# Kernel optimization log

Hardware: AMD Instinct MI355X
Metric: run time of the kernel (lower is better)

## Reference

```python
import jax, jax.numpy as jnp
import numpy as np
from jax import lax

K, E, HID, NH, L = 512, 256, 512, 8, 2
N, S1, S2, C, U, V, W = 2, 8, 9, 3, 8, 8, 8
S = S1 + S2 - 1  # 16, matches sum(cfg['seq_length']) - 1


def setup_inputs() -> dict:
    key = jax.random.key(0)
    ks = iter(jax.random.split(key, 40))
    g = lambda shape, s=0.02: jax.random.normal(next(ks), shape, jnp.float32) * s
    inp = {
        'code': jax.random.randint(next(ks), (N, S1, C, U, V, W), 0, K),
        'ncode': jax.random.randint(next(ks), (N, S2, C, U, V, W), 0, K),
        'emb': g((K, E)), 'pos_emb': g((S, E)),
        'Wq': g((L, 3, 3, 3, E, E)), 'bq': g((L, E)),
        'Wk': g((L, 3, 3, 3, E, E)), 'bk': g((L, E)),
        'Wv': g((L, 3, 3, 3, E, E)), 'bv': g((L, E)),
        'Wo': g((L, 3, 3, 3, E, E)), 'bo': g((L, E)),
        'ln1_g': jnp.ones((L, E)), 'ln1_b': jnp.zeros((L, E)),
        'ln2_g': jnp.ones((L, E)), 'ln2_b': jnp.zeros((L, E)),
        'Wc1': g((L, 3, 3, 3, E, HID)), 'bc1': g((L, HID)),
        'Wc2': g((L, 3, 3, 3, HID, E)), 'bc2': g((L, E)),
        'cls_W1': g((E, E)), 'cls_b1': jnp.zeros((E,)),
        'cls_ln_g': jnp.ones((E,)), 'cls_ln_b': jnp.zeros((E,)),
        'cls_W2': g((E, K)), 'cls_b2': jnp.zeros((K,)),
    }
    return inp


def _conv3d(t, w, b):
    # t: [B, S, U, V, W, Cin]; conv with kernel 3, stride 1, pad 1 (SAME)
    B_, S_, U_, V_, W_, Ci = t.shape
    y = lax.conv_general_dilated(t.reshape(B_ * S_, U_, V_, W_, Ci), w, (1, 1, 1), 'SAME',
                                 dimension_numbers=('NDHWC', 'DHWIO', 'NDHWC')) + b
    return y.reshape(B_, S_, U_, V_, W_, -1)


def _ln(t, g, b):
    mu = t.mean(-1, keepdims=True)
    var = ((t - mu) ** 2).mean(-1, keepdims=True)
    return (t - mu) * lax.rsqrt(var + 1e-5) * g + b


def _forward(code, ncode, emb, pos_emb, Wq, bq, Wk, bk, Wv, bv, Wo, bo,
             ln1_g, ln1_b, ln2_g, ln2_b, Wc1, bc1, Wc2, bc2,
             cls_W1, cls_b1, cls_ln_g, cls_ln_b, cls_W2, cls_b2):
    x = jnp.concatenate([code, ncode[:, :-1]], axis=1)  # [N, S, C, U, V, W]
    n, s, c, u, v, w = x.shape
    s2 = ncode.shape[1]
    x = x.transpose(0, 2, 1, 3, 4, 5).reshape(n * c, s, u, v, w)
    h = emb[x] + pos_emb[:s][None, :, None, None, None, :]  # [B, S, U, V, W, E]
    e = h.shape[-1]
    d = e // NH
    scale = jnp.asarray(d, h.dtype) ** 0.5
    # causal mask with first seq_length[0] columns fully visible
    m = jnp.tril(jnp.ones((s, s), bool)).at[:, :S1].set(True)

    def heads(t):
        return t.reshape(t.shape[0], s, u, v, w, NH, d).transpose(0, 5, 2, 3, 4, 1, 6)

    for i in range(Wq.shape[0]):
        q = heads(_conv3d(h, Wq[i], bq[i]))
        kk = heads(_conv3d(h, Wk[i], bk[i]))
        vv = heads(_conv3d(h, Wv[i], bv[i]))
        scores = jnp.einsum('bnuvwsd,bnuvwtd->bnuvwst', q, kk) / scale
        scores = jnp.where(m, scores, jnp.asarray(-1e30, scores.dtype))
        attn = jax.nn.softmax(scores, axis=-1)
        o = jnp.einsum('bnuvwst,bnuvwtd->bnuvwsd', attn, vv)
        o = o.transpose(0, 5, 2, 3, 4, 1, 6).reshape(h.shape[0], s, u, v, w, e)
        o = _conv3d(o, Wo[i], bo[i])
        h = _ln(h + o, ln1_g[i], ln1_b[i])
        f = _conv3d(jax.nn.gelu(_conv3d(h, Wc1[i], bc1[i]), approximate=False), Wc2[i], bc2[i])
        h = _ln(h + f, ln2_g[i], ln2_b[i])

    h = h[:, -s2:]
    h = h.reshape(n, c, s2, u, v, w, e).transpose(0, 2, 1, 3, 4, 5, 6)  # [N, S2, C, U, V, W, E]
    z = jnp.einsum('...e,ef->...f', h, cls_W1) + cls_b1
    z = jax.nn.gelu(_ln(z, cls_ln_g, cls_ln_b), approximate=False)
    z = jnp.einsum('...e,ek->...k', z, cls_W2) + cls_b2
    score = z.transpose(0, 6, 1, 2, 3, 4, 5)  # [N, K, S2, C, U, V, W]
    return score


def reference(code, ncode, emb, pos_emb, Wq, bq, Wk, bk, Wv, bv, Wo, bo,
              ln1_g, ln1_b, ln2_g, ln2_b, Wc1, bc1, Wc2, bc2,
              cls_W1, cls_b1, cls_ln_g, cls_ln_b, cls_W2, cls_b2):
    score = _forward(code, ncode, emb, pos_emb, Wq, bq, Wk, bk, Wv, bv, Wo, bo,
                     ln1_g, ln1_b, ln2_g, ln2_b, Wc1, bc1, Wc2, bc2,
                     cls_W1, cls_b1, cls_ln_g, cls_ln_b, cls_W2, cls_b2)
    logp = jax.nn.log_softmax(score, axis=1)
    nll = -jnp.take_along_axis(logp, ncode[:, None], axis=1)[:, 0]
    loss = nll.mean()
    pred = jnp.argmax(score, axis=1)
    return score, loss, pred
```

## Files before the change

kernel.cpp:

```cpp
#include <hip/hip_runtime.h>


typedef _Float16 f16;
typedef __attribute__((ext_vector_type(8))) _Float16 f16x8;
typedef __attribute__((ext_vector_type(4))) _Float16 f16x4;
typedef __attribute__((ext_vector_type(4))) float f32x4;

static constexpr long kSC = 14155776;
static constexpr float kDS = 4.8828125e-4f;

#define MFMA16(a, b, c) __builtin_amdgcn_mfma_f32_16x16x32_f16((a), (b), (c), 0, 0, 0)

__device__ __forceinline__ void gl16(const void* g, void* l) {
  __builtin_amdgcn_global_load_lds((const __attribute__((address_space(1))) void*)g,
                                   (__attribute__((address_space(3))) void*)l,
                                   16, 0, 0);
}

__device__ __forceinline__ float wave_sum_f(float x) {
#pragma unroll
  for (int m = 32; m; m >>= 1) x += __shfl_xor(x, m);
  return x;
}

__device__ __forceinline__ void split2(float x, f16* h, f16* l) {
  f16 hh = (f16)x;
  *h = hh;
  *l = (f16)((x - (float)hh) * 2048.0f);
}

__device__ __forceinline__ float rec2(f16 h, f16 l) {
  return (float)h + (float)l * kDS;
}

__device__ __forceinline__ float gelu_exact(float x) {
  return 0.5f * x * (1.0f + erff(x * 0.70710678118654752f));
}

__global__ __launch_bounds__(256) void wsplit_kernel(
    const float* __restrict__ src, f16* __restrict__ hi, f16* __restrict__ lo,
    int G, int Ci, int Co, int CoTot, int co0) {
  long n = (long)G * Ci * Co;
  long i = (long)blockIdx.x * 256 + threadIdx.x;
  if (i >= n) return;
  int co = (int)(i % Co);
  long t = i / Co;
  int ci = (int)(t % Ci);
  int g  = (int)(t / Ci);
  float x = src[i];
  long o = ((long)g * CoTot + co0 + co) * Ci + ci;
  split2(x, hi + o, lo + o);
}

__global__ __launch_bounds__(256) void bpack_kernel(
    const float* __restrict__ bq, const float* __restrict__ bk,
    const float* __restrict__ bv, float* __restrict__ dst) {
  int i = blockIdx.x * 256 + threadIdx.x;
  if (i < 256) dst[i] = bq[i];
  else if (i < 512) dst[i] = bk[i - 256];
  else if (i < 768) dst[i] = bv[i - 512];
}

__global__ __launch_bounds__(256) void embed_kernel(
    const int* __restrict__ code, const int* __restrict__ ncode,
    const float* __restrict__ emb, const float* __restrict__ pos,
    f16* __restrict__ Hh, f16* __restrict__ Hl) {
  int tok = blockIdx.x;
  int e = threadIdx.x;
  int g = tok >> 13;
  int rem = tok & 8191;
  int s = rem >> 9;
  int vox = rem & 511;
  int n = g / 3, c = g - 3 * n;
  int idx;
  if (s < 8) idx = code[((n * 8 + s) * 3 + c) * 512 + vox];
  else       idx = ncode[((n * 9 + (s - 8)) * 3 + c) * 512 + vox];
  float val = emb[idx * 256 + e] + pos[s * 256 + e];
  long o = (long)tok * 256 + e;
  split2(val, Hh + o, Hl + o);
}

template <int CIN, int COUTT, int ACT, int RESID>
__global__ __launch_bounds__(256, 2) void conv8_kernel(
    const f16* __restrict__ Xh, const f16* __restrict__ Xl, long xz_s, int xr,
    const f16* __restrict__ Wh, const f16* __restrict__ Wl,
    const float* __restrict__ bias,
    f16* __restrict__ Yh, f16* __restrict__ Yl, long yz_s, int yr, int nz) {
  constexpr int KB = CIN / 32;
  constexpr int NY = COUTT / 128;
  __shared__ __align__(16) f16 lsAll[40960];

  const int nwg = 64 * NY * nz;
  const int q = nwg >> 3;
  const int bid = blockIdx.x;
  const int wg = (bid & 7) * q + (bid >> 3);
  const int y = wg / (64 * nz);
  const int rem = wg - y * (64 * nz);
  const int z = rem >> 6;
  const int mt = rem & 63;
  const int img = mt >> 2, up = mt & 3;
  const int u0 = up * 2;
  const int coutb0 = y * 128;

  const int tid = threadIdx.x;
  const int wid = tid >> 6, lane = tid & 63;
  const int wm = wid >> 1, wn = wid & 1;
  const int l15 = lane & 15, lk = lane >> 4;

  const long xz = (long)z * xz_s;
  const long yz = (long)z * yz_s;

  f32x4 aA[4][4], aB[4][4];
#pragma unroll
  for (int mf = 0; mf < 4; ++mf)
#pragma unroll
    for (int nf = 0; nf < 4; ++nf) {
      float bv = bias[coutb0 + wn * 64 + nf * 16 + l15];
      aA[mf][nf] = (f32x4){bv, bv, bv, bv};
      aB[mf][nf] = (f32x4){0.f, 0.f, 0.f, 0.f};
    }

  const int swrow = tid >> 2;
  const int sswz = (tid & 3) ^ ((tid >> 3) & 3);

  auto stageA = [&](int kb) {
#pragma unroll
    for (int j = 0; j < 4; ++j) {
      const int uu = u0 - 1 + j;
      if (uu < 0 || uu >= 8) continue;
      const long g = xz + ((long)(img * 512 + uu * 64 + swrow)) * (long)xr
                     + kb * 32 + sswz * 8;
      gl16(Xh + g, &lsAll[j * 2048 + tid * 8]);
      gl16(Xl + g, &lsAll[8192 + j * 2048 + tid * 8]);
    }
  };
  auto stageB = [&](int o, int kb, int buf) {
    const int wb = 16384 + buf * 8192;
#pragma unroll
    for (int i = 0; i < 2; ++i) {
      const long g = ((long)o * COUTT + coutb0 + i * 64 + swrow) * (long)CIN
                     + kb * 32 + sswz * 8;
      gl16(Wh + g, &lsAll[wb + i * 2048 + tid * 8]);
      gl16(Wl + g, &lsAll[wb + 4096 + i * 2048 + tid * 8]);
    }
  };
  auto compute = [&](int o, int buf) {
    const int du = o / 9 - 1, dv = (o / 3) % 3 - 1, dw = o % 3 - 1;
    const int gu = u0 + wm + du;
    if ((unsigned)gu >= 8u) return;
    const int p = wm + 1 + du;
    const int wb = 16384 + buf * 8192;
    f16x8 bh[4], bl[4];
#pragma unroll
    for (int nf = 0; nf < 4; ++nf) {
      const int rb = wn * 64 + nf * 16 + l15;
      const int sw = lk ^ ((rb >> 1) & 3);
      bh[nf] = *(const f16x8*)&lsAll[wb + rb * 32 + sw * 8];
      bl[nf] = *(const f16x8*)&lsAll[wb + 4096 + rb * 32 + sw * 8];
    }
    __builtin_amdgcn_s_setprio(1);
#pragma unroll
    for (int mf = 0; mf < 4; ++mf) {
      const int vrow = mf * 16 + l15;
      const int vv = (vrow >> 3) + dv, ww = (vrow & 7) + dw;
      const bool ok = ((unsigned)vv < 8u) && ((unsigned)ww < 8u);
      f16x8 ah = {0, 0, 0, 0, 0, 0, 0, 0};
      f16x8 al = {0, 0, 0, 0, 0, 0, 0, 0};
      if (ok) {
        const int lrow = p * 64 + vv * 8 + ww;
        const int sw = lk ^ ((lrow >> 1) & 3);
        ah = *(const f16x8*)&lsAll[lrow * 32 + sw * 8];
        al = *(const f16x8*)&lsAll[8192 + lrow * 32 + sw * 8];
      }
#pragma unroll
      for (int nf = 0; nf < 4; ++nf) {
        aA[mf][nf] = MFMA16(ah, bh[nf], aA[mf][nf]);
        aB[mf][nf] = MFMA16(ah, bl[nf], aB[mf][nf]);
        aB[mf][nf] = MFMA16(al, bh[nf], aB[mf][nf]);
      }
    }
    __builtin_amdgcn_s_setprio(0);
  };

  stageA(0);
  stageB(0, 0, 0);

  int bcur = 0;
#pragma unroll 1
  for (int kb = 0; kb < KB; ++kb) {
#pragma unroll 1
    for (int o = 0; o < 27; ++o) {
      int bnext = bcur + 1; if (bnext == 3) bnext = 0;
      const bool haveNext = !(o == 26 && kb + 1 == KB);
      if (o < 26)           stageB(o + 1, kb, bnext);
      else if (kb + 1 < KB) stageB(0, kb + 1, bnext);
      if (haveNext) asm volatile("s_waitcnt vmcnt(4)\n\ts_barrier" ::: "memory");
      else          asm volatile("s_waitcnt vmcnt(0)\n\ts_barrier" ::: "memory");
      compute(o, bcur);
      if (o == 26 && kb + 1 < KB) {
        asm volatile("s_barrier" ::: "memory");
        stageA(kb + 1);
      }
      bcur = bnext;
    }
  }
  __syncthreads();

  float* sY = (float*)lsAll;
#pragma unroll 1
  for (int rh = 0; rh < 2; ++rh) {
    if (wm == rh) {
#pragma unroll
      for (int mf = 0; mf < 4; ++mf)
#pragma unroll
        for (int nf = 0; nf < 4; ++nf)
#pragma unroll
          for (int j = 0; j < 4; ++j) {
            const int row = mf * 16 + lk * 4 + j;
            const int col = wn * 64 + nf * 16 + l15;
            sY[row * 132 + col] = aA[mf][nf][j] + aB[mf][nf][j] * kDS;
          }
    }
    __syncthreads();
#pragma unroll
    for (int it = 0; it < 2; ++it) {
      const int row = it * 32 + (tid >> 3);
      const int c0 = (tid & 7) * 16;
      const long grow = (long)img * 512 + (u0 + rh) * 64 + row;
      const long gidx = yz + grow * (long)yr + coutb0 + c0;
      float yv[16];
#pragma unroll
      for (int i2 = 0; i2 < 16; ++i2) yv[i2] = sY[row * 132 + c0 + i2];
      if (ACT) {
#pragma unroll
        for (int i2 = 0; i2 < 16; ++i2) yv[i2] = gelu_exact(yv[i2]);
      }
      if (RESID) {
        f16x8 r0h = *(const f16x8*)&Yh[gidx];
        f16x8 r1h = *(const f16x8*)&Yh[gidx + 8];
        f16x8 r0l = *(const f16x8*)&Yl[gidx];
        f16x8 r1l = *(const f16x8*)&Yl[gidx + 8];
#pragma unroll
        for (int i2 = 0; i2 < 8; ++i2) {
          yv[i2] += rec2(r0h[i2], r0l[i2]);
          yv[8 + i2] += rec2(r1h[i2], r1l[i2]);
        }
      }
      f16x8 h0, h1, l0, l1;
#pragma unroll
      for (int i2 = 0; i2 < 8; ++i2) {
        f16 a, b;
        split2(yv[i2], &a, &b); h0[i2] = a; l0[i2] = b;
        split2(yv[8 + i2], &a, &b); h1[i2] = a; l1[i2] = b;
      }
      if (RESID) {
        *(f16x8*)&Yh[gidx] = h0;
        *(f16x8*)&Yh[gidx + 8] = h1;
        *(f16x8*)&Yl[gidx] = l0;
        *(f16x8*)&Yl[gidx + 8] = l1;
      } else {
        __builtin_nontemporal_store(h0, (f16x8*)&Yh[gidx]);
        __builtin_nontemporal_store(h1, (f16x8*)&Yh[gidx + 8]);
        __builtin_nontemporal_store(l0, (f16x8*)&Yl[gidx]);
        __builtin_nontemporal_store(l1, (f16x8*)&Yl[gidx + 8]);
      }
    }
    __syncthreads();
  }
}

template <int K_, int COUT, bool F32OUT>
__global__ __launch_bounds__(256) void gemm_kernel(
    const f16* __restrict__ Xh, const f16* __restrict__ Xl,
    const f16* __restrict__ Wh, const f16* __restrict__ Wl,
    const float* __restrict__ bias,
    f16* __restrict__ Yh, f16* __restrict__ Yl, float* __restrict__ Yf) {
  const int m0 = blockIdx.x * 64;
  const int coutb = blockIdx.y * 64;
  const int tid = threadIdx.x;
  const int wid = tid >> 6, lane = tid & 63;
  const int l15 = lane & 15, lk = lane >> 4;
  const int arow = m0 + wid * 16 + l15;

  f32x4 accA[4], accB[4];
#pragma unroll
  for (int cg = 0; cg < 4; ++cg) {
    float bv = bias[coutb + cg * 16 + l15];
    accA[cg] = (f32x4){bv, bv, bv, bv};
    accB[cg] = (f32x4){0.f, 0.f, 0.f, 0.f};
  }
  const f16* pah = Xh + (long)arow * K_ + lk * 8;
  const f16* pal = Xl + (long)arow * K_ + lk * 8;
  const f16* pbh = Wh + ((long)coutb + l15) * K_ + lk * 8;
  const f16* pbl = Wl + ((long)coutb + l15) * K_ + lk * 8;
#pragma unroll 2
  for (int kb = 0; kb < K_ / 32; ++kb) {
    f16x8 ah = *(const f16x8*)(pah + kb * 32);
    f16x8 al = *(const f16x8*)(pal + kb * 32);
#pragma unroll
    for (int cg = 0; cg < 4; ++cg) {
      f16x8 bh = *(const f16x8*)(pbh + (long)cg * 16 * K_ + kb * 32);
      f16x8 bl = *(const f16x8*)(pbl + (long)cg * 16 * K_ + kb * 32);
      accA[cg] = MFMA16(ah, bh, accA[cg]);
      accB[cg] = MFMA16(ah, bl, accB[cg]);
      accB[cg] = MFMA16(al, bh, accB[cg]);
    }
  }
  const long ybase = ((long)m0 + wid * 16) * (long)COUT + coutb;
#pragma unroll
  for (int cg = 0; cg < 4; ++cg)
#pragma unroll
    for (int j = 0; j < 4; ++j) {
      int r = lk * 4 + j;
      float y = accA[cg][j] + accB[cg][j] * kDS;
      long idx = ybase + (long)r * COUT + cg * 16 + l15;
      if (F32OUT) Yf[idx] = y;
      else        split2(y, Yh + idx, Yl + idx);
    }
}

__global__ __launch_bounds__(256) void attn_kernel(
    f16* __restrict__ QKVh, f16* __restrict__ QKVl) {
  __shared__ float sq[4][16][33];
  __shared__ float sk[4][16][33];
  __shared__ float sv[4][16][33];
  __shared__ float ss[4][16][17];
  const int wid = threadIdx.x >> 6, lane = threadIdx.x & 63;
  const int p = blockIdx.x * 4 + wid;
  const int cs = p >> 12;
  const int loc = p & 4095;
  const int nh = loc >> 9;
  const int vox = loc & 511;
  const int srow = lane >> 2;
  const int dp = (lane & 3) * 8;
  const long sbase = (long)cs * 6291456;
  const long base = sbase + ((long)(srow * 512 + vox)) * 768 + nh * 32 + dp;

  {
    f16x8 qh = *(const f16x8*)(QKVh + base);
    f16x8 ql = *(const f16x8*)(QKVl + base);
    f16x8 kh = *(const f16x8*)(QKVh + base + 256);
    f16x8 kl = *(const f16x8*)(QKVl + base + 256);
    f16x8 vh = *(const f16x8*)(QKVh + base + 512);
    f16x8 vl = *(const f16x8*)(QKVl + base + 512);
#pragma unroll
    for (int j = 0; j < 8; ++j) {
      sq[wid][srow][dp + j] = rec2(qh[j], ql[j]);
      sk[wid][srow][dp + j] = rec2(kh[j], kl[j]);
      sv[wid][srow][dp + j] = rec2(vh[j], vl[j]);
    }
  }
  __syncthreads();
#pragma unroll
  for (int pp = 0; pp < 4; ++pp) {
    int pr = lane * 4 + pp;
    int qi = pr >> 4, kt = pr & 15;
    float s = 0.f;
#pragma unroll
    for (int d = 0; d < 32; ++d) s += sq[wid][qi][d] * sk[wid][kt][d];
    bool allowed = (kt < 8) || (kt <= qi);
    ss[wid][qi][kt] = allowed ? s * 0.17677669529663687f : -1e30f;
  }
  __syncthreads();
  if (lane < 16) {
    float m = -1e30f;
#pragma unroll
    for (int t = 0; t < 16; ++t) m = fmaxf(m, ss[wid][lane][t]);
    float ex[16];
    float sum = 0.f;
#pragma unroll
    for (int t = 0; t < 16; ++t) { ex[t] = expf(ss[wid][lane][t] - m); sum += ex[t]; }
    float inv = 1.0f / sum;
#pragma unroll
    for (int t = 0; t < 16; ++t) ss[wid][lane][t] = ex[t] * inv;
  }
  __syncthreads();
  float o[8] = {0, 0, 0, 0, 0, 0, 0, 0};
#pragma unroll
  for (int t = 0; t < 16; ++t) {
    float a = ss[wid][srow][t];
#pragma unroll
    for (int j = 0; j < 8; ++j) o[j] += a * sv[wid][t][dp + j];
  }
#pragma unroll
  for (int j = 0; j < 8; ++j) split2(o[j], QKVh + base + j, QKVl + base + j);
}

__global__ __launch_bounds__(256) void ln_kernel(
    f16* __restrict__ Hh, f16* __restrict__ Hl,
    const float* __restrict__ gam, const float* __restrict__ bet) {
  const int wid = threadIdx.x >> 6, lane = threadIdx.x & 63;
  const long tok = (long)blockIdx.x * 4 + wid;
  const long base = tok * 256 + lane * 4;
  f16x4 hh = *(const f16x4*)(Hh + base);
  f16x4 hl = *(const f16x4*)(Hl + base);
  float v0 = rec2(hh[0], hl[0]), v1 = rec2(hh[1], hl[1]);
  float v2 = rec2(hh[2], hl[2]), v3 = rec2(hh[3], hl[3]);
  float mu = wave_sum_f(v0 + v1 + v2 + v3) * (1.0f / 256.0f);
  float d0 = v0 - mu, d1 = v1 - mu, d2 = v2 - mu, d3 = v3 - mu;
  float var = wave_sum_f(d0 * d0 + d1 * d1 + d2 * d2 + d3 * d3) * (1.0f / 256.0f);
  float rs = rsqrtf(var + 1e-5f);
  float4 gv = *(const float4*)(gam + lane * 4);
  float4 bv = *(const float4*)(bet + lane * 4);
  float y0 = d0 * rs * gv.x + bv.x, y1 = d1 * rs * gv.y + bv.y;
  float y2 = d2 * rs * gv.z + bv.z, y3 = d3 * rs * gv.w + bv.w;
  f16x4 oh, ol;
  f16 a, b2;
  split2(y0, &a, &b2); oh[0] = a; ol[0] = b2;
  split2(y1, &a, &b2); oh[1] = a; ol[1] = b2;
  split2(y2, &a, &b2); oh[2] = a; ol[2] = b2;
  split2(y3, &a, &b2); oh[3] = a; ol[3] = b2;
  *(f16x4*)(Hh + base) = oh;
  *(f16x4*)(Hl + base) = ol;
}

__global__ __launch_bounds__(256) void ln_gelu_kernel(
    f16* __restrict__ Zh, f16* __restrict__ Zl,
    const float* __restrict__ gam, const float* __restrict__ bet) {
  const int wid = threadIdx.x >> 6, lane = threadIdx.x & 63;
  const long tok = (long)blockIdx.x * 4 + wid;
  const long base = tok * 256 + lane * 4;
  f16x4 hh = *(const f16x4*)(Zh + base);
  f16x4 hl = *(const f16x4*)(Zl + base);
  float v0 = rec2(hh[0], hl[0]), v1 = rec2(hh[1], hl[1]);
  float v2 = rec2(hh[2], hl[2]), v3 = rec2(hh[3], hl[3]);
  float mu = wave_sum_f(v0 + v1 + v2 + v3) * (1.0f / 256.0f);
  float d0 = v0 - mu, d1 = v1 - mu, d2 = v2 - mu, d3 = v3 - mu;
  float var = wave_sum_f(d0 * d0 + d1 * d1 + d2 * d2 + d3 * d3) * (1.0f / 256.0f);
  float rs = rsqrtf(var + 1e-5f);
  float4 gv = *(const float4*)(gam + lane * 4);
  float4 bv = *(const float4*)(bet + lane * 4);
  float y0 = gelu_exact(d0 * rs * gv.x + bv.x);
  float y1 = gelu_exact(d1 * rs * gv.y + bv.y);
  float y2 = gelu_exact(d2 * rs * gv.z + bv.z);
  float y3 = gelu_exact(d3 * rs * gv.w + bv.w);
  f16x4 oh, ol;
  f16 a, b2;
  split2(y0, &a, &b2); oh[0] = a; ol[0] = b2;
  split2(y1, &a, &b2); oh[1] = a; ol[1] = b2;
  split2(y2, &a, &b2); oh[2] = a; ol[2] = b2;
  split2(y3, &a, &b2); oh[3] = a; ol[3] = b2;
  *(f16x4*)(Zh + base) = oh;
  *(f16x4*)(Zl + base) = ol;
}

__global__ __launch_bounds__(256) void gather_kernel(
    const f16* __restrict__ Hh, const f16* __restrict__ Hl, int n,
    f16* __restrict__ Xh, f16* __restrict__ Xl) {
  const int tc = blockIdx.x;
  const int e = threadIdx.x;
  const int s2 = tc / 1536;
  int r = tc - s2 * 1536;
  const int c = r >> 9;
  const int vox = r & 511;
  const int g = n * 3 + c;
  const int s = 7 + s2;
  const long src = ((long)(g * 16 + s) * 512 + vox) * 256 + e;
  const long dst = (long)tc * 256 + e;
  Xh[dst] = Hh[src];
  Xl[dst] = Hl[src];
}

__global__ __launch_bounds__(256) void transpose_kernel(
    const float* __restrict__ Z2, float* __restrict__ out) {
  __shared__ float tile[32][33];
  const int t0 = blockIdx.x * 32;
  const int k0 = blockIdx.y * 32;
  const int tx = threadIdx.x & 31;
  const int ty = threadIdx.x >> 5;
#pragma unroll
  for (int i = 0; i < 32; i += 8)
    tile[ty + i][tx] = Z2[((long)(t0 + ty + i)) * 512 + k0 + tx];
  __syncthreads();
#pragma unroll
  for (int i = 0; i < 32; i += 8)
    out[((long)(k0 + ty + i)) * 13824 + t0 + tx] = tile[tx][ty + i];
}

__global__ __launch_bounds__(256) void loss_pred_kernel(
    const float* __restrict__ Z2, const int* __restrict__ ncode,
    float* __restrict__ pred, float* __restrict__ partial) {
  __shared__ float sh[4];
  const int wid = threadIdx.x >> 6, lane = threadIdx.x & 63;
  const int tok = blockIdx.x * 4 + wid;
  const float* row = Z2 + (long)tok * 512;
  float4 a = *(const float4*)(row + lane * 8);
  float4 b = *(const float4*)(row + lane * 8 + 4);
  float vals[8] = {a.x, a.y, a.z, a.w, b.x, b.y, b.z, b.w};
  float mx = vals[0];
  int mi = lane * 8;
#pragma unroll
  for (int j = 1; j < 8; ++j)
    if (vals[j] > mx) { mx = vals[j]; mi = lane * 8 + j; }
#pragma unroll
  for (int m = 1; m < 64; m <<= 1) {
    float ox = __shfl_xor(mx, m);
    int oi = __shfl_xor(mi, m);
    if (ox > mx || (ox == mx && oi < mi)) { mx = ox; mi = oi; }
  }
  float se = 0.f;
#pragma unroll
  for (int j = 0; j < 8; ++j) se += expf(vals[j] - mx);
  se = wave_sum_f(se);
  if (lane == 0) {
    int tgt = ncode[tok];
    float nll = mx + logf(se) - row[tgt];
    pred[tok] = (float)mi;
    sh[wid] = nll;
  }
  __syncthreads();
  if (threadIdx.x == 0) partial[blockIdx.x] = sh[0] + sh[1] + sh[2] + sh[3];
}

__global__ __launch_bounds__(256) void loss_final_kernel(
    const float* __restrict__ partial, float* __restrict__ out) {
  __shared__ float sh[4];
  float s = 0.f;
  for (int i = threadIdx.x; i < 6912; i += 256) s += partial[i];
  s = wave_sum_f(s);
  if ((threadIdx.x & 63) == 0) sh[threadIdx.x >> 6] = s;
  __syncthreads();
  if (threadIdx.x == 0) out[0] = (sh[0] + sh[1] + sh[2] + sh[3]) * (1.0f / 27648.0f);
}

__global__ __launch_bounds__(256) void fill_kernel(float* __restrict__ p, long n, float v) {
  long i = (long)blockIdx.x * 256 + threadIdx.x;
  if (i < n) p[i] = v;
}

extern "C" void kernel_launch(void* const* d_in, const int* in_sizes, int n_in,
                              void* d_out, int out_size, void* d_ws, size_t ws_size,
                              hipStream_t stream) {
  const int* code   = (const int*)d_in[0];
  const int* ncode  = (const int*)d_in[1];
  const float* emb  = (const float*)d_in[2];
  const float* pos  = (const float*)d_in[3];
  const float* Wq   = (const float*)d_in[4];
  const float* bq   = (const float*)d_in[5];
  const float* Wk   = (const float*)d_in[6];
  const float* bk   = (const float*)d_in[7];
  const float* Wv   = (const float*)d_in[8];
  const float* bv   = (const float*)d_in[9];
  const float* Wo   = (const float*)d_in[10];
  const float* bo   = (const float*)d_in[11];
  const float* ln1g = (const float*)d_in[12];
  const float* ln1b = (const float*)d_in[13];
  const float* ln2g = (const float*)d_in[14];
  const float* ln2b = (const float*)d_in[15];
  const float* Wc1  = (const float*)d_in[16];
  const float* bc1  = (const float*)d_in[17];
  const float* Wc2  = (const float*)d_in[18];
  const float* bc2  = (const float*)d_in[19];
  const float* cW1  = (const float*)d_in[20];
  const float* cb1  = (const float*)d_in[21];
  const float* clng = (const float*)d_in[22];
  const float* clnb = (const float*)d_in[23];
  const float* cW2  = (const float*)d_in[24];
  const float* cb2  = (const float*)d_in[25];
  float* out = (float*)d_out;
  (void)in_sizes; (void)n_in; (void)out_size;

  const long WSLOT = 5308416;
  const long HSL   = 2097152;
  const long QSL   = 6291456;
  const long T1SL  = 4194304;
  const long CLMIN = 21233664;

  auto needf = [&](int ns) -> size_t {
    long slab = (long)ns * 2 * QSL;
    if (slab < CLMIN) slab = CLMIN;
    return (size_t)(2 * WSLOT + 2 * 12582912L + slab) * 2 + 6912 * 4 + 768 * 4 + 4096;
  };
  int NS = 0;
  if      (ws_size >= needf(6)) NS = 6;
  else if (ws_size >= needf(3)) NS = 3;
  else if (ws_size >= needf(2)) NS = 2;
  else if (ws_size >= needf(1)) NS = 1;
  if (NS == 0) {
    fill_kernel<<<dim3(109), 256, 0, stream>>>(out + kSC, 27649, -1.0f);
    return;
  }
  long slab_f16 = (long)NS * 2 * QSL;
  if (slab_f16 < CLMIN) slab_f16 = CLMIN;

  f16* wh = (f16*)d_ws;
  f16* wl = wh + WSLOT;
  f16* Hh = wl + WSLOT;
  f16* Hl = Hh + 12582912;
  f16* S  = Hl + 12582912;
  float* partial = (float*)(S + slab_f16);
  float* bcat = partial + 6912;

  const size_t WQKVO = 27u * 256 * 256;
  const size_t WC1SZ = 27u * 256 * 512;
  const size_t WC2SZ = 27u * 512 * 256;

  embed_kernel<<<dim3(49152), 256, 0, stream>>>(code, ncode, emb, pos, Hh, Hl);

  const int nchunk = 6 / NS;
  f16* qkvh = S;
  f16* qkvl = S + (long)NS * QSL;
  f16* t1h  = S;
  f16* t1l  = S + (long)NS * T1SL;

  for (int l = 0; l < 2; ++l) {
    const float* wq = Wq + (size_t)l * WQKVO;
    const float* wk = Wk + (size_t)l * WQKVO;
    const float* wv = Wv + (size_t)l * WQKVO;
    const float* wo = Wo + (size_t)l * WQKVO;
    const float* wc1 = Wc1 + (size_t)l * WC1SZ;
    const float* wc2 = Wc2 + (size_t)l * WC2SZ;
    bpack_kernel<<<dim3(3), 256, 0, stream>>>(bq + l * 256, bk + l * 256, bv + l * 256, bcat);
    for (int ch = 0; ch < nchunk; ++ch) {
      f16* Xh = Hh + (long)ch * NS * HSL;
      f16* Xl = Hl + (long)ch * NS * HSL;
      wsplit_kernel<<<dim3(6912), 256, 0, stream>>>(wq, wh, wl, 27, 256, 256, 768, 0);
      wsplit_kernel<<<dim3(6912), 256, 0, stream>>>(wk, wh, wl, 27, 256, 256, 768, 256);
      wsplit_kernel<<<dim3(6912), 256, 0, stream>>>(wv, wh, wl, 27, 256, 256, 768, 512);
      conv8_kernel<256, 768, 0, 0><<<dim3(64 * 6 * NS), 256, 0, stream>>>(
          Xh, Xl, HSL, 256, wh, wl, bcat, qkvh, qkvl, QSL, 768, NS);
      attn_kernel<<<dim3(NS * 1024), 256, 0, stream>>>(qkvh, qkvl);
      wsplit_kernel<<<dim3(6912), 256, 0, stream>>>(wo, wh, wl, 27, 256, 256, 256, 0);
      conv8_kernel<256, 256, 0, 1><<<dim3(64 * 2 * NS), 256, 0, stream>>>(
          qkvh, qkvl, QSL, 768, wh, wl, bo + l * 256, Xh, Xl, HSL, 256, NS);
      ln_kernel<<<dim3(2048 * NS), 256, 0, stream>>>(Xh, Xl, ln1g + l * 256, ln1b + l * 256);
      wsplit_kernel<<<dim3(13824), 256, 0, stream>>>(wc1, wh, wl, 27, 256, 512, 512, 0);
      conv8_kernel<256, 512, 1, 0><<<dim3(64 * 4 * NS), 256, 0, stream>>>(
          Xh, Xl, HSL, 256, wh, wl, bc1 + l * 512, t1h, t1l, T1SL, 512, NS);
      wsplit_kernel<<<dim3(13824), 256, 0, stream>>>(wc2, wh, wl, 27, 512, 256, 256, 0);
      conv8_kernel<512, 256, 0, 1><<<dim3(64 * 2 * NS), 256, 0, stream>>>(
          t1h, t1l, T1SL, 512, wh, wl, bc2 + l * 256, Xh, Xl, HSL, 256, NS);
      ln_kernel<<<dim3(2048 * NS), 256, 0, stream>>>(Xh, Xl, ln2g + l * 256, ln2b + l * 256);
    }
  }

  for (int n = 0; n < 2; ++n) {
    f16* Z1h = S;
    f16* Z1l = S + 3538944;
    f16* Xch = S + 7077888;
    f16* Xcl = S + 10616832;
    float* Z2 = (float*)(S + 7077888);
    gather_kernel<<<dim3(13824), 256, 0, stream>>>(Hh, Hl, n, Xch, Xcl);
    wsplit_kernel<<<dim3(256), 256, 0, stream>>>(cW1, wh, wl, 1, 256, 256, 256, 0);
    gemm_kernel<256, 256, false><<<dim3(216, 4), 256, 0, stream>>>(Xch, Xcl, wh, wl, cb1, Z1h, Z1l, nullptr);
    ln_gelu_kernel<<<dim3(3456), 256, 0, stream>>>(Z1h, Z1l, clng, clnb);
    wsplit_kernel<<<dim3(512), 256, 0, stream>>>(cW2, wh, wl, 1, 256, 512, 512, 0);
    gemm_kernel<256, 512, true><<<dim3(216, 8), 256, 0, stream>>>(Z1h, Z1l, wh, wl, cb2, nullptr, nullptr, Z2);
    transpose_kernel<<<dim3(432, 16), 256, 0, stream>>>(Z2, out + (long)n * 512 * 13824);
    loss_pred_kernel<<<dim3(3456), 256, 0, stream>>>(Z2, ncode + n * 13824,
                                                     out + kSC + 1 + n * 13824, partial + n * 3456);
  }
  loss_final_kernel<<<dim3(1), 256, 0, stream>>>(partial, out + kSC);
}
```

Before: 7.604 ms.

## Switch conv kernel to 32x32x16 MFMA and double-buffered weight staging

The 3D conv kernel now uses 32x32x16 f16 MFMA tiles (2x2 fragments per wave, two K sub-steps) instead of 16x16x32 tiles, which reduces fragment loads and instruction count per output. The weight pipeline drops from a triple buffer with a manual vmcnt wait plus barrier to a double buffer with __syncthreads after each offset, shrinking LDS use. The simpler synchronisation may expose more load latency, since the next stage's loads only get one compute step to land before the barrier.

After: 8.085 ms. +6.3%, slower.

```diff
diff --git a/kernel.cpp b/kernel.cpp
--- a/kernel.cpp
+++ b/kernel.cpp
@@ -5,11 +5,13 @@
 typedef __attribute__((ext_vector_type(8))) _Float16 f16x8;
 typedef __attribute__((ext_vector_type(4))) _Float16 f16x4;
 typedef __attribute__((ext_vector_type(4))) float f32x4;
+typedef __attribute__((ext_vector_type(16))) float f32x16;
 
 static constexpr long kSC = 14155776;
 static constexpr float kDS = 4.8828125e-4f;
 
 #define MFMA16(a, b, c) __builtin_amdgcn_mfma_f32_16x16x32_f16((a), (b), (c), 0, 0, 0)
+#define MFMA32(a, b, c) __builtin_amdgcn_mfma_f32_32x32x16_f16((a), (b), (c), 0, 0, 0)
 
 __device__ __forceinline__ void gl16(const void* g, void* l) {
   __builtin_amdgcn_global_load_lds((const __attribute__((address_space(1))) void*)g,
@@ -81,14 +83,14 @@
 }
 
 template <int CIN, int COUTT, int ACT, int RESID>
-__global__ __launch_bounds__(256, 2) void conv8_kernel(
+__global__ __launch_bounds__(256, 2) void conv10_kernel(
     const f16* __restrict__ Xh, const f16* __restrict__ Xl, long xz_s, int xr,
     const f16* __restrict__ Wh, const f16* __restrict__ Wl,
     const float* __restrict__ bias,
     f16* __restrict__ Yh, f16* __restrict__ Yl, long yz_s, int yr, int nz) {
   constexpr int KB = CIN / 32;
   constexpr int NY = COUTT / 128;
-  __shared__ __align__(16) f16 lsAll[40960];
+  __shared__ __align__(16) f16 lsAll[32768];
 
   const int nwg = 64 * NY * nz;
   const int q = nwg >> 3;
@@ -105,19 +107,19 @@
   const int tid = threadIdx.x;
   const int wid = tid >> 6, lane = tid & 63;
   const int wm = wid >> 1, wn = wid & 1;
-  const int l15 = lane & 15, lk = lane >> 4;
+  const int l31 = lane & 31, s5 = lane >> 5;
 
   const long xz = (long)z * xz_s;
   const long yz = (long)z * yz_s;
 
-  f32x4 aA[4][4], aB[4][4];
-#pragma unroll
-  for (int mf = 0; mf < 4; ++mf)
-#pragma unroll
-    for (int nf = 0; nf < 4; ++nf) {
-      float bv = bias[coutb0 + wn * 64 + nf * 16 + l15];
-      aA[mf][nf] = (f32x4){bv, bv, bv, bv};
-      aB[mf][nf] = (f32x4){0.f, 0.f, 0.f, 0.f};
+  f32x16 aA[2][2], aB[2][2];
+#pragma unroll
+  for (int mf = 0; mf < 2; ++mf)
+#pragma unroll
+    for (int nf = 0; nf < 2; ++nf) {
+      float bv = bias[coutb0 + wn * 64 + nf * 32 + l31];
+#pragma unroll
+      for (int j = 0; j < 16; ++j) { aA[mf][nf][j] = bv; aB[mf][nf][j] = 0.f; }
     }
 
   const int swrow = tid >> 2;
@@ -150,33 +152,41 @@
     if ((unsigned)gu >= 8u) return;
     const int p = wm + 1 + du;
     const int wb = 16384 + buf * 8192;
-    f16x8 bh[4], bl[4];
-#pragma unroll
-    for (int nf = 0; nf < 4; ++nf) {
-      const int rb = wn * 64 + nf * 16 + l15;
-      const int sw = lk ^ ((rb >> 1) & 3);
-      bh[nf] = *(const f16x8*)&lsAll[wb + rb * 32 + sw * 8];
-      bl[nf] = *(const f16x8*)&lsAll[wb + 4096 + rb * 32 + sw * 8];
+    f16x8 bh[2][2], bl[2][2];
+#pragma unroll
+    for (int nf = 0; nf < 2; ++nf) {
+      const int rb = wn * 64 + nf * 32 + l31;
+      const int rsw = (rb >> 1) & 3;
+#pragma unroll
+      for (int ks = 0; ks < 2; ++ks) {
+        const int sl = (ks * 2 + s5) ^ rsw;
+        bh[nf][ks] = *(const f16x8*)&lsAll[wb + rb * 32 + sl * 8];
+        bl[nf][ks] = *(const f16x8*)&lsAll[wb + 4096 + rb * 32 + sl * 8];
+      }
     }
     __builtin_amdgcn_s_setprio(1);
 #pragma unroll
-    for (int mf = 0; mf < 4; ++mf) {
-      const int vrow = mf * 16 + l15;
+    for (int mf = 0; mf < 2; ++mf) {
+      const int vrow = mf * 32 + l31;
       const int vv = (vrow >> 3) + dv, ww = (vrow & 7) + dw;
       const bool ok = ((unsigned)vv < 8u) && ((unsigned)ww < 8u);
-      f16x8 ah = {0, 0, 0, 0, 0, 0, 0, 0};
-      f16x8 al = {0, 0, 0, 0, 0, 0, 0, 0};
-      if (ok) {
-        const int lrow = p * 64 + vv * 8 + ww;
-        const int sw = lk ^ ((lrow >> 1) & 3);
-        ah = *(const f16x8*)&lsAll[lrow * 32 + sw * 8];
-        al = *(const f16x8*)&lsAll[8192 + lrow * 32 + sw * 8];
-      }
-#pragma unroll
-      for (int nf = 0; nf < 4; ++nf) {
-        aA[mf][nf] = MFMA16(ah, bh[nf], aA[mf][nf]);
-        aB[mf][nf] = MFMA16(ah, bl[nf], aB[mf][nf]);
-        aB[mf][nf] = MFMA16(al, bh[nf], aB[mf][nf]);
+      const int lrow = p * 64 + vv * 8 + ww;
+      const int asw = (lrow >> 1) & 3;
+#pragma unroll
+      for (int ks = 0; ks < 2; ++ks) {
+        f16x8 ah = {0, 0, 0, 0, 0, 0, 0, 0};
+        f16x8 al = {0, 0, 0, 0, 0, 0, 0, 0};
+        if (ok) {
+          const int sl = (ks * 2 + s5) ^ asw;
+          ah = *(const f16x8*)&lsAll[lrow * 32 + sl * 8];
+          al = *(const f16x8*)&lsAll[8192 + lrow * 32 + sl * 8];
+        }
+#pragma unroll
+        for (int nf = 0; nf < 2; ++nf) {
+          aA[mf][nf] = MFMA32(ah, bh[nf][ks], aA[mf][nf]);
+          aB[mf][nf] = MFMA32(ah, bl[nf][ks], aB[mf][nf]);
+          aB[mf][nf] = MFMA32(al, bh[nf][ks], aB[mf][nf]);
+        }
       }
     }
     __builtin_amdgcn_s_setprio(0);
@@ -184,40 +194,37 @@
 
   stageA(0);
   stageB(0, 0, 0);
-
-  int bcur = 0;
+  __syncthreads();
+
+  int cur = 0;
 #pragma unroll 1
   for (int kb = 0; kb < KB; ++kb) {
 #pragma unroll 1
     for (int o = 0; o < 27; ++o) {
-      int bnext = bcur + 1; if (bnext == 3) bnext = 0;
-      const bool haveNext = !(o == 26 && kb + 1 == KB);
-      if (o < 26)           stageB(o + 1, kb, bnext);
-      else if (kb + 1 < KB) stageB(0, kb + 1, bnext);
-      if (haveNext) asm volatile("s_waitcnt vmcnt(4)\n\ts_barrier" ::: "memory");
-      else          asm volatile("s_waitcnt vmcnt(0)\n\ts_barrier" ::: "memory");
-      compute(o, bcur);
-      if (o == 26 && kb + 1 < KB) {
-        asm volatile("s_barrier" ::: "memory");
-        stageA(kb + 1);
-      }
-      bcur = bnext;
-    }
-  }
-  __syncthreads();
+      if (o < 26)           stageB(o + 1, kb, cur ^ 1);
+      else if (kb + 1 < KB) stageB(0, kb + 1, cur ^ 1);
+      compute(o, cur);
+      __syncthreads();
+      cur ^= 1;
+    }
+    if (kb + 1 < KB) {
+      stageA(kb + 1);
+      __syncthreads();
+    }
+  }
 
   float* sY = (float*)lsAll;
 #pragma unroll 1
   for (int rh = 0; rh < 2; ++rh) {
     if (wm == rh) {
 #pragma unroll
-      for (int mf = 0; mf < 4; ++mf)
-#pragma unroll
-        for (int nf = 0; nf < 4; ++nf)
-#pragma unroll
-          for (int j = 0; j < 4; ++j) {
-            const int row = mf * 16 + lk * 4 + j;
-            const int col = wn * 64 + nf * 16 + l15;
+      for (int mf = 0; mf < 2; ++mf)
+#pragma unroll
+        for (int nf = 0; nf < 2; ++nf)
+#pragma unroll
+          for (int j = 0; j < 16; ++j) {
+            const int row = mf * 32 + (j & 3) + 8 * (j >> 2) + 4 * s5;
+            const int col = wn * 64 + nf * 32 + l31;
             sY[row * 132 + col] = aA[mf][nf][j] + aB[mf][nf][j] * kDS;
           }
     }
@@ -617,18 +624,18 @@
       wsplit_kernel<<<dim3(6912), 256, 0, stream>>>(wq, wh, wl, 27, 256, 256, 768, 0);
       wsplit_kernel<<<dim3(6912), 256, 0, stream>>>(wk, wh, wl, 27, 256, 256, 768, 256);
       wsplit_kernel<<<dim3(6912), 256, 0, stream>>>(wv, wh, wl, 27, 256, 256, 768, 512);
-      conv8_kernel<256, 768, 0, 0><<<dim3(64 * 6 * NS), 256, 0, stream>>>(
+      conv10_kernel<256, 768, 0, 0><<<dim3(64 * 6 * NS), 256, 0, stream>>>(
           Xh, Xl, HSL, 256, wh, wl, bcat, qkvh, qkvl, QSL, 768, NS);
       attn_kernel<<<dim3(NS * 1024), 256, 0, stream>>>(qkvh, qkvl);
       wsplit_kernel<<<dim3(6912), 256, 0, stream>>>(wo, wh, wl, 27, 256, 256, 256, 0);
-      conv8_kernel<256, 256, 0, 1><<<dim3(64 * 2 * NS), 256, 0, stream>>>(
+      conv10_kernel<256, 256, 0, 1><<<dim3(64 * 2 * NS), 256, 0, stream>>>(
           qkvh, qkvl, QSL, 768, wh, wl, bo + l * 256, Xh, Xl, HSL, 256, NS);
       ln_kernel<<<dim3(2048 * NS), 256, 0, stream>>>(Xh, Xl, ln1g + l * 256, ln1b + l * 256);
       wsplit_kernel<<<dim3(13824), 256, 0, stream>>>(wc1, wh, wl, 27, 256, 512, 512, 0);
-      conv8_kernel<256, 512, 1, 0><<<dim3(64 * 4 * NS), 256, 0, stream>>>(
+      conv10_kernel<256, 512, 1, 0><<<dim3(64 * 4 * NS), 256, 0, stream>>>(
           Xh, Xl, HSL, 256, wh, wl, bc1 + l * 512, t1h, t1l, T1SL, 512, NS);
       wsplit_kernel<<<dim3(13824), 256, 0, stream>>>(wc2, wh, wl, 27, 512, 256, 256, 0);
-      conv8_kernel<512, 256, 0, 1><<<dim3(64 * 2 * NS), 256, 0, stream>>>(
+      conv10_kernel<512, 256, 0, 1><<<dim3(64 * 2 * NS), 256, 0, stream>>>(
           t1h, t1l, T1SL, 512, wh, wl, bc2 + l * 256, Xh, Xl, HSL, 256, NS);
       ln_kernel<<<dim3(2048 * NS), 256, 0, stream>>>(Xh, Xl, ln2g + l * 256, ln2b + l * 256);
     }
```
